# Optimization experiments

Measured on AMD Instinct MI355X. Metric: run time of the kernel, lower is better.

The kernel has to match this reference:

```python
import jax, jax.numpy as jnp
from jax import lax
import numpy as np

IMG_H, IMG_W = 800.0, 1344.0
NMS_PRE, NMS_POST, MAX_NUM = 2000, 1000, 1000
IOU_THR = 0.7
STRIDES = [4, 8, 16, 32, 64]
SIZES = [(200, 336), (100, 168), (50, 84), (25, 42), (13, 21)]
MAX_RATIO = float(abs(np.log(16.0 / 1000.0)))  # mmdet wh_ratio_clip


def _make_anchors(H, W, stride):
    # mmdet AnchorGenerator: scales=[8], ratios=[0.5,1,2], base_size=stride
    ratios = np.array([0.5, 1.0, 2.0])
    scale = 8.0
    hr = np.sqrt(ratios)
    wr = 1.0 / hr
    ws = stride * wr * scale
    hs = stride * hr * scale
    c = stride / 2.0
    base = np.stack([c - 0.5 * ws, c - 0.5 * hs, c + 0.5 * ws, c + 0.5 * hs], 1)  # [3,4]
    xx, yy = np.meshgrid(np.arange(W) * stride, np.arange(H) * stride)
    shifts = np.stack([xx, yy, xx, yy], -1).reshape(-1, 1, 4)  # [H*W,1,4]
    return (shifts + base[None]).reshape(-1, 4).astype(np.float32)  # order (H,W,A)


def setup_inputs() -> dict:
    key = jax.random.key(0)
    inp = {}
    for i, (H, W) in enumerate(SIZES):
        k1, k2, key = jax.random.split(key, 3)
        inp[f"cls{i}"] = jax.random.normal(k1, (2, 3, H, W), jnp.float32)
        inp[f"bbox{i}"] = jax.random.normal(k2, (2, 12, H, W), jnp.float32) * 0.5
        inp[f"anc{i}"] = jnp.asarray(_make_anchors(H, W, STRIDES[i]))
    return inp


def _delta2bbox(deltas, anchors):
    # deltas, anchors: [..., 4]; means=0, stds=1
    dx, dy = deltas[..., 0], deltas[..., 1]
    dw = jnp.clip(deltas[..., 2], -MAX_RATIO, MAX_RATIO)
    dh = jnp.clip(deltas[..., 3], -MAX_RATIO, MAX_RATIO)
    pw = anchors[..., 2] - anchors[..., 0]
    ph = anchors[..., 3] - anchors[..., 1]
    px = (anchors[..., 0] + anchors[..., 2]) * 0.5
    py = (anchors[..., 1] + anchors[..., 3]) * 0.5
    gw = pw * jnp.exp(dw)
    gh = ph * jnp.exp(dh)
    gx = px + pw * dx
    gy = py + ph * dy
    x1 = jnp.clip(gx - 0.5 * gw, 0.0, IMG_W)
    y1 = jnp.clip(gy - 0.5 * gh, 0.0, IMG_H)
    x2 = jnp.clip(gx + 0.5 * gw, 0.0, IMG_W)
    y2 = jnp.clip(gy + 0.5 * gh, 0.0, IMG_H)
    return jnp.stack([x1, y1, x2, y2], axis=-1)


def _pairwise_iou(b):
    # b: [N,4]
    area = (b[:, 2] - b[:, 0]) * (b[:, 3] - b[:, 1])
    lt = jnp.maximum(b[:, None, :2], b[None, :, :2])
    rb = jnp.minimum(b[:, None, 2:], b[None, :, 2:])
    wh = jnp.clip(rb - lt, 0.0, None)
    inter = wh[..., 0] * wh[..., 1]
    union = area[:, None] + area[None, :] - inter
    return inter / jnp.maximum(union, 1e-6)


def _nms_single(boxes, scores):
    # boxes [NMS_PRE,4], scores [NMS_PRE] (one image). Greedy NMS, keep NMS_POST.
    N = scores.shape[0]
    order = jnp.argsort(-scores)
    b = boxes[order]
    s = scores[order]
    iou = _pairwise_iou(lax.stop_gradient(b))
    idx = jnp.arange(N)

    def step(supp, i):
        keep_i = jnp.logical_not(supp[i])
        supp = supp | (keep_i & (iou[i] > IOU_THR) & (idx > i))
        return supp, keep_i

    _, keeps = lax.scan(step, jnp.zeros((N,), bool), idx)
    s_kept = jnp.where(keeps, s, -1.0)
    top_s, top_i = lax.top_k(s_kept, NMS_POST)
    return b[top_i], top_s


def _process_level(cls, bbox, anchors):
    B = cls.shape[0]
    # [B,A,H,W] -> [B,H,W,A] -> [B,N]; [B,A*4,H,W] -> [B,H,W,A*4] -> [B,N,4]
    scores = jax.nn.sigmoid(cls.transpose(0, 2, 3, 1).reshape(B, -1))
    deltas = bbox.transpose(0, 2, 3, 1).reshape(B, -1, 4)
    N = scores.shape[1]
    if N < NMS_PRE:  # pad small levels to min_num_bboxes (nms_pre)
        pad = NMS_PRE - N
        scores = jnp.pad(scores, ((0, 0), (0, pad)), constant_values=-1.0)
        deltas = jnp.pad(deltas, ((0, 0), (0, pad), (0, 0)))
        anchors = jnp.pad(anchors, ((0, pad), (0, 0)))
        top_s = scores
        top_i = jnp.broadcast_to(jnp.arange(NMS_PRE), (B, NMS_PRE))
    else:
        top_s, top_i = lax.top_k(scores, NMS_PRE)
    deltas_g = jnp.take_along_axis(deltas, top_i[..., None], axis=1)  # [B,NMS_PRE,4]
    anc_g = anchors[top_i]  # [B,NMS_PRE,4]
    props = _delta2bbox(deltas_g, anc_g)
    boxes, sc = jax.vmap(_nms_single)(props, top_s)
    return sc, boxes


def _forward(cls_list, bbox_list, anc_list):
    mlvl_scores, mlvl_props = [], []
    for cls, bbox, anc in zip(cls_list, bbox_list, anc_list):
        s, p = _process_level(cls, bbox, anc)
        mlvl_scores.append(s)
        mlvl_props.append(p)
    scores = jnp.concatenate(mlvl_scores, axis=1)      # [B, 5*NMS_POST]
    proposals = jnp.concatenate(mlvl_props, axis=1)    # [B, 5*NMS_POST, 4]
    _, topk_inds = lax.top_k(scores, MAX_NUM)
    return jnp.take_along_axis(proposals, topk_inds[..., None], axis=1)  # [B, MAX_NUM, 4]


def reference(cls0, cls1, cls2, cls3, cls4,
              bbox0, bbox1, bbox2, bbox3, bbox4,
              anc0, anc1, anc2, anc3, anc4):
    return _forward([cls0, cls1, cls2, cls3, cls4],
                    [bbox0, bbox1, bbox2, bbox3, bbox4],
                    [anc0, anc1, anc2, anc3, anc4])
```

## Files before the change

kernel.cpp:

```cpp
#include <hip/hip_runtime.h>
#include <cmath>


#define NPRE 2000
#define NPOST 1000

static __device__ __forceinline__ unsigned int flipf_dev(float f) {
  unsigned int u = __float_as_uint(f);
  return (u & 0x80000000u) ? ~u : (u | 0x80000000u);
}
static __device__ __forceinline__ float unflipf_dev(unsigned int k) {
  unsigned int u = (k & 0x80000000u) ? (k ^ 0x80000000u) : ~k;
  return __uint_as_float(u);
}
static __device__ __forceinline__ unsigned long long flip64_dev(double d) {
  unsigned long long u = (unsigned long long)__double_as_longlong(d);
  return (u & 0x8000000000000000ull) ? ~u : (u | 0x8000000000000000ull);
}

struct RPNParams {
  const float* cls[5];
  const float* bbox[5];
  const float* anc[5];
  unsigned int* hist;
  unsigned int* histT;
  unsigned int* mainCount;
  unsigned int* candCount;
  unsigned int* Bstar;
  unsigned long long* mainEK;
  unsigned long long* candEK;
  unsigned long long* ekG;
  unsigned int* partialR;
  double* selBoxes;
  double* selScores;
  unsigned long long* mask;
  double* postScores;
  float* postBoxes;
  unsigned int* partial;
  float* out;
};

__device__ __constant__ int c_NL[5]  = {201600, 50400, 12600, 3150, 819};
__device__ __constant__ int c_HW[5]  = {67200, 16800, 4200, 1050, 273};
__device__ __constant__ int c_BPT[8] = {99, 99, 25, 25, 7, 7, 2, 2};
__device__ __constant__ int c_BPT12[8] = {25, 25, 7, 7, 2, 2, 1, 1};
__device__ __constant__ int c_HSTART[8] = {0, 25, 50, 57, 64, 66, 68, 69};

static __device__ __forceinline__ void map_block(int bx, int& t, int& chunk) {
  int start = 0;
  t = 0;
  for (int k = 0; k < 8; k++) {
    if (bx < start + c_BPT[k]) { t = k; break; }
    start += c_BPT[k];
  }
  chunk = bx - start;
}
static __device__ __forceinline__ void map_block12(int bx, int& t, int& chunk) {
  int start = 0;
  t = 0;
  for (int k = 0; k < 8; k++) {
    if (bx < start + c_BPT12[k]) { t = k; break; }
    start += c_BPT12[k];
  }
  chunk = bx - start;
}

__global__ __launch_bounds__(1024) void k_hist(RPNParams p) {
  __shared__ unsigned int lh[16384];
  int t, chunk;
  map_block12(blockIdx.x, t, chunk);
  int l = t >> 1, b = t & 1;
  int N = c_NL[l], HW = c_HW[l];
  const float* cls = p.cls[l] + (size_t)b * 3 * HW;
  int tid = threadIdx.x;
  for (int i = tid; i < 16384; i += 1024) lh[i] = 0;
  __syncthreads();
  int base = chunk * 8192 + tid;
#pragma unroll
  for (int k = 0; k < 8; k++) {
    int n = base + k * 1024;
    if (n < N) {
      int a = n % 3, hw = n / 3;
      unsigned int key = flipf_dev(cls[a * HW + hw]);
      atomicAdd(&lh[key >> 18], 1u);
    }
  }
  __syncthreads();
  unsigned int* hout = p.hist + (size_t)blockIdx.x * 16384;
  for (int i = tid; i < 16384; i += 1024) hout[i] = lh[i];
}

__global__ __launch_bounds__(1024) void k_hred(RPNParams p) {
  int t = blockIdx.x >> 4;
  int slice = blockIdx.x & 15;
  int bin = slice * 1024 + threadIdx.x;
  int start = c_HSTART[t];
  int bpt = c_BPT12[t];
  unsigned int s0 = 0, s1 = 0, s2 = 0, s3 = 0;
  int bb = 0;
  for (; bb + 4 <= bpt; bb += 4) {
    s0 += p.hist[(size_t)(start + bb + 0) * 16384 + bin];
    s1 += p.hist[(size_t)(start + bb + 1) * 16384 + bin];
    s2 += p.hist[(size_t)(start + bb + 2) * 16384 + bin];
    s3 += p.hist[(size_t)(start + bb + 3) * 16384 + bin];
  }
  for (; bb < bpt; bb++) s0 += p.hist[(size_t)(start + bb) * 16384 + bin];
  p.histT[(size_t)t * 16384 + bin] = s0 + s1 + s2 + s3;
}

__global__ __launch_bounds__(1024) void k_find(RPNParams p) {
  int t = blockIdx.x;
  __shared__ unsigned int H[16384];
  __shared__ unsigned int S[1024];
  __shared__ int gsel;
  __shared__ unsigned int baseAbove;
  int tid = threadIdx.x;
  const unsigned int* hT = p.histT + (size_t)t * 16384;
  for (int bin = tid; bin < 16384; bin += 1024) H[bin] = hT[bin];
  __syncthreads();
  {
    unsigned int s = 0;
#pragma unroll
    for (int k = 0; k < 16; k++) s += H[tid * 16 + k];
    S[tid] = s;
  }
  __syncthreads();
  for (int off = 1; off < 1024; off <<= 1) {
    unsigned int add = (tid + off < 1024) ? S[tid + off] : 0u;
    __syncthreads();
    S[tid] += add;
    __syncthreads();
  }
  const unsigned int need = NPRE;
  if (S[tid] >= need && (tid == 1023 || S[tid + 1] < need)) {
    gsel = tid;
    baseAbove = (tid == 1023) ? 0u : S[tid + 1];
  }
  __syncthreads();
  if (tid == 0) {
    int gg = gsel;
    unsigned int c = baseAbove;
    int bstar = gg * 16;
    for (int bb = 15; bb >= 0; bb--) {
      c += H[gg * 16 + bb];
      if (c >= need) { bstar = gg * 16 + bb; break; }
    }
    p.Bstar[t] = (unsigned int)bstar;
  }
}

__global__ void k_compact(RPNParams p) {
  int t, chunk;
  map_block(blockIdx.x, t, chunk);
  int l = t >> 1, b = t & 1;
  int N = c_NL[l], HW = c_HW[l];
  const float* cls = p.cls[l] + (size_t)b * 3 * HW;
  unsigned int Bs = p.Bstar[t];
  int base = chunk * 2048 + threadIdx.x;
  for (int k = 0; k < 2; k++) {
    int n = base + k * 1024;
    if (n < N) {
      int a = n % 3, hw = n / 3;
      unsigned int key = flipf_dev(cls[a * HW + hw]);
      unsigned int hi = key >> 18;
      unsigned long long ek =
          ((unsigned long long)key << 32) | (unsigned int)(~(unsigned int)n);
      if (hi > Bs) {
        unsigned int pos = atomicAdd(&p.mainCount[t], 1u);
        if (pos < 2048u) p.mainEK[(size_t)t * 2048 + pos] = ek;
      } else if (hi == Bs) {
        unsigned int pos = atomicAdd(&p.candCount[t], 1u);
        if (pos < 8192u) p.candEK[(size_t)t * 8192 + pos] = ek;
      }
    }
  }
}

__global__ void k_fill(RPNParams p) {
  int t = blockIdx.x;
  int l = t >> 1, b = t & 1;
  int N = c_NL[l], HW = c_HW[l];
  int tid = threadIdx.x;
  unsigned long long* ekG = p.ekG + (size_t)t * 2048;
  if (N >= NPRE) {
    unsigned int cGT = min(p.mainCount[t], 2000u);
    unsigned int nC = min(p.candCount[t], 8192u);
    unsigned int needIn = 2000u - cGT;
    for (unsigned int m = tid; m < cGT; m += 256)
      ekG[m] = p.mainEK[(size_t)t * 2048 + m];
    const unsigned long long* cek = p.candEK + (size_t)t * 8192;
    for (unsigned int e = tid; e < nC; e += 256) {
      unsigned long long ve = cek[e];
      unsigned int r = 0;
      for (unsigned int j = 0; j < nC; j++) r += (cek[j] > ve) ? 1u : 0u;
      if (r < needIn) ekG[cGT + r] = ve;
    }
    for (unsigned int r2 = 2000u + tid; r2 < 2048u; r2 += 256)
      ekG[r2] = (unsigned long long)(unsigned int)(~r2);
  } else {
    const float* cls = p.cls[l] + (size_t)b * 3 * HW;
    for (int r = tid; r < 2048; r += 256) {
      if (r < N) {
        int a = r % 3, hw = r / 3;
        unsigned int key = flipf_dev(cls[a * HW + hw]);
        ekG[r] = ((unsigned long long)key << 32) |
                 (unsigned int)(~(unsigned int)r);
      } else {
        ekG[r] = (unsigned long long)(unsigned int)(~(unsigned int)r);
      }
    }
  }
}

__global__ void k_rank(RPNParams p) {
  int t = blockIdx.x >> 3;
  int s = blockIdx.x & 7;
  int tid = threadIdx.x;
  __shared__ unsigned long long sl[256];
  const unsigned long long* ekG = p.ekG + (size_t)t * 2048;
  sl[tid] = ekG[s * 256 + tid];
  __syncthreads();
  unsigned long long ve[8];
  unsigned int r[8];
#pragma unroll
  for (int k = 0; k < 8; k++) {
    ve[k] = ekG[k * 256 + tid];
    r[k] = 0;
  }
  for (int j = 0; j < 256; j++) {
    unsigned long long vj = sl[j];
#pragma unroll
    for (int k = 0; k < 8; k++) r[k] += (vj > ve[k]) ? 1u : 0u;
  }
  unsigned int* out = p.partialR + ((size_t)t * 8 + s) * 2048;
#pragma unroll
  for (int k = 0; k < 8; k++) out[k * 256 + tid] = r[k];
}

__global__ void k_scatter(RPNParams p) {
  int t = blockIdx.x;
  int l = t >> 1, b = t & 1;
  int HW = c_HW[l];
  int tid = threadIdx.x;
  __shared__ unsigned long long srt[2048];
  const unsigned long long* ekG = p.ekG + (size_t)t * 2048;
  for (int e = tid; e < 2048; e += 1024) {
    unsigned int rk = 0;
#pragma unroll
    for (int s = 0; s < 8; s++)
      rk += p.partialR[((size_t)t * 8 + s) * 2048 + e];
    srt[rk] = ekG[e];
  }
  __syncthreads();

  const double RCLIP = fabs(log(16.0 / 1000.0));
  const float* bbx = p.bbox[l] + (size_t)b * 12 * HW;
  const float* anc = p.anc[l];
  for (int r = tid; r < NPRE; r += 1024) {
    unsigned long long v = srt[r];
    unsigned int key = (unsigned int)(v >> 32);
    double* SB = p.selBoxes + ((size_t)t * NPRE + r) * 4;
    if (key == 0u) {
      SB[0] = 0.0; SB[1] = 0.0; SB[2] = 0.0; SB[3] = 0.0;
      p.selScores[(size_t)t * NPRE + r] = -1.0;
    } else {
      unsigned int idx = ~(unsigned int)(v & 0xFFFFFFFFull);
      int a = (int)(idx % 3u);
      int hw = (int)(idx / 3u);
      double d0 = (double)bbx[(a * 4 + 0) * HW + hw];
      double d1 = (double)bbx[(a * 4 + 1) * HW + hw];
      double d2 = (double)bbx[(a * 4 + 2) * HW + hw];
      double d3 = (double)bbx[(a * 4 + 3) * HW + hw];
      double a0 = (double)anc[(size_t)idx * 4 + 0];
      double a1 = (double)anc[(size_t)idx * 4 + 1];
      double a2 = (double)anc[(size_t)idx * 4 + 2];
      double a3 = (double)anc[(size_t)idx * 4 + 3];
      double dw = fmin(fmax(d2, -RCLIP), RCLIP);
      double dh = fmin(fmax(d3, -RCLIP), RCLIP);
      double pw = a2 - a0, ph = a3 - a1;
      double px = (a0 + a2) * 0.5, py = (a1 + a3) * 0.5;
      double gw = pw * exp(dw), gh = ph * exp(dh);
      double gx = px + pw * d0, gy = py + ph * d1;
      double x1 = fmin(fmax(gx - 0.5 * gw, 0.0), 1344.0);
      double y1 = fmin(fmax(gy - 0.5 * gh, 0.0), 800.0);
      double x2 = fmin(fmax(gx + 0.5 * gw, 0.0), 1344.0);
      double y2 = fmin(fmax(gy + 0.5 * gh, 0.0), 800.0);
      SB[0] = x1; SB[1] = y1; SB[2] = x2; SB[3] = y2;
      float f = unflipf_dev(key);
      p.selScores[(size_t)t * NPRE + r] = 1.0 / (1.0 + exp(-(double)f));
    }
  }
}

__global__ __launch_bounds__(640) void k_iou(RPNParams p) {
  int bx = blockIdx.x;
  int t = bx / 25;
  int q = bx % 25;
  __shared__ float X1[2048], Y1[2048], X2[2048], Y2[2048], AR[2048];
  const double* SB = p.selBoxes + (size_t)t * NPRE * 4;
  for (int i = threadIdx.x; i < 2048; i += 640) {
    float x1 = 0.f, y1 = 0.f, x2 = 0.f, y2 = 0.f;
    if (i < NPRE) {
      x1 = (float)SB[i * 4 + 0]; y1 = (float)SB[i * 4 + 1];
      x2 = (float)SB[i * 4 + 2]; y2 = (float)SB[i * 4 + 3];
    }
    X1[i] = x1; Y1[i] = y1; X2[i] = x2; Y2[i] = y2;
    AR[i] = (x2 - x1) * (y2 - y1);
  }
  __syncthreads();
  int wave = threadIdx.x >> 6, lane = threadIdx.x & 63;
  int g = q + 25 * wave;
  int i0 = g * 8;
  float x1i[8], y1i[8], x2i[8], y2i[8], ai[8];
#pragma unroll
  for (int r = 0; r < 8; r++) {
    int i = i0 + r;
    x1i[r] = X1[i]; y1i[r] = Y1[i]; x2i[r] = X2[i]; y2i[r] = Y2[i];
    ai[r] = AR[i];
  }
  int c0 = i0 >> 6;
  int j0 = c0 * 64 + lane;
  float cx1 = X1[j0], cy1 = Y1[j0], cx2 = X2[j0], cy2 = Y2[j0], car = AR[j0];
  for (int k = c0; k < 32; k++) {
    float nx1 = 0.f, ny1 = 0.f, nx2 = 0.f, ny2 = 0.f, nar = 0.f;
    if (k + 1 < 32) {
      int jn = (k + 1) * 64 + lane;
      nx1 = X1[jn]; ny1 = Y1[jn]; nx2 = X2[jn]; ny2 = Y2[jn];
      nar = AR[jn];
    }
    int j = k * 64 + lane;
    bool jin = j < NPRE;
    bool pred[8], need[8];
    bool needAny = false;
#pragma unroll
    for (int r = 0; r < 8; r++) {
      int i = i0 + r;
      bool valid = jin && (j > i);
      float lx = fmaxf(x1i[r], cx1), ly = fmaxf(y1i[r], cy1);
      float rx = fminf(x2i[r], cx2), ry = fminf(y2i[r], cy2);
      float w = fmaxf(rx - lx, 0.0f), h = fmaxf(ry - ly, 0.0f);
      float inter = w * h;
      float uni = fmaxf(ai[r] + car - inter, 1e-6f);
      float diff = inter - 0.7f * uni;
      pred[r] = valid && (diff > 0.0f);
      need[r] = valid && (fabsf(diff) <= 4.0f + 1e-5f * uni);
      needAny |= need[r];
    }
    if (__any(needAny)) {
#pragma unroll
      for (int r = 0; r < 8; r++) {
        if (need[r]) {
          int i = i0 + r;
          double a0 = SB[i * 4 + 0], b0 = SB[i * 4 + 1];
          double a2 = SB[i * 4 + 2], b2 = SB[i * 4 + 3];
          double c0d = SB[j * 4 + 0], d0 = SB[j * 4 + 1];
          double c2 = SB[j * 4 + 2], d2 = SB[j * 4 + 3];
          double dai = (a2 - a0) * (b2 - b0);
          double daj = (c2 - c0d) * (d2 - d0);
          double lxd = fmax(a0, c0d), lyd = fmax(b0, d0);
          double rxd = fmin(a2, c2), ryd = fmin(b2, d2);
          double wd = fmax(rxd - lxd, 0.0), hd = fmax(ryd - lyd, 0.0);
          double interd = wd * hd;
          double unid = fmax(dai + daj - interd, 1e-6);
          pred[r] = (interd / unid) > 0.7;
        }
      }
    }
#pragma unroll
    for (int r = 0; r < 8; r++) {
      unsigned long long word = __ballot(pred[r]);
      if (lane == 0) p.mask[((size_t)t * NPRE + i0 + r) * 32 + k] = word;
    }
    cx1 = nx1; cy1 = ny1; cx2 = nx2; cy2 = ny2; car = nar;
  }
}

#define GRP_N 63
#define RING 6
__global__ __launch_bounds__(256) void k_greedy(RPNParams p) {
  int t = blockIdx.x;
  int tid = threadIdx.x;
  __shared__ unsigned long long ring[RING * 1024];
  __shared__ int ready[GRP_N];
  __shared__ int cons_s;
  __shared__ unsigned long long kw[32], aw[32], bw[32];
  __shared__ unsigned int prefA[33], prefB[33];
  volatile int* rdy = ready;
  volatile int* cons = &cons_s;
  const unsigned long long* MK = p.mask + (size_t)t * NPRE * 32;
  for (int i = tid; i < GRP_N; i += 256) ready[i] = 0;
  if (tid == 0) cons_s = 0;
  __syncthreads();

  int wave = tid >> 6, lane = tid & 63;
  if (wave >= 1) {
    for (int g = wave - 1; g < GRP_N; g += 3) {
      while (g - *cons >= RING) __builtin_amdgcn_s_sleep(1);
      unsigned long long v[16];
#pragma unroll
      for (int k = 0; k < 16; k++) {
        int idx = k * 64 + lane;
        int row = g * 32 + (idx >> 5);
        v[k] = (row < NPRE) ? MK[(size_t)row * 32 + (idx & 31)] : 0ull;
      }
      int slot = g % RING;
#pragma unroll
      for (int k = 0; k < 16; k++)
        ring[slot * 1024 + k * 64 + lane] = v[k];
      __threadfence_block();
      if (lane == 0) rdy[g] = 1;
    }
  } else {
    unsigned long long supp = 0ull, keep = 0ull;
    auto doGroup = [&](int g, int base) {
      while (rdy[g] == 0) { }
      __threadfence_block();
      int slot = g % RING;
      int c = g >> 1;
      unsigned long long rv[32];
#pragma unroll
      for (int r = 0; r < 32; r++)
        rv[r] = ring[slot * 1024 + r * 32 + (lane & 31)];
      unsigned int sh = (unsigned int)(supp >> base);
      unsigned int s32 = (unsigned int)__builtin_amdgcn_readlane((int)sh, c);
      unsigned int kg = 0;
#pragma unroll
      for (int r = 0; r < 32; r++) {
        unsigned int rvh = (unsigned int)(rv[r] >> base);
        bool kp = (s32 & (1u << r)) == 0u;
        kg |= kp ? (1u << r) : 0u;
        s32 |= kp ? rvh : 0u;
      }
      kg = (unsigned int)__builtin_amdgcn_readlane((int)kg, c);
#pragma unroll
      for (int r = 0; r < 32; r++) {
        if (kg & (1u << r)) supp |= rv[r];
      }
      keep |= (lane == c) ? ((unsigned long long)kg << base) : 0ull;
      __threadfence_block();
      if (lane == 63) *cons = g + 1;
    };
    for (int g = 0; g + 1 < GRP_N; g += 2) {
      doGroup(g, 0);
      doGroup(g + 1, 32);
    }
    doGroup(GRP_N - 1, 0);
    if (lane < 32) kw[lane] = keep;
  }
  __syncthreads();

  for (int ch = wave; ch < 32; ch += 4) {
    int i = ch * 64 + lane;
    bool inr = i < NPRE;
    bool kb = inr && ((kw[ch] >> lane) & 1ull);
    bool A = kb && (inr ? (p.selScores[(size_t)t * NPRE + i] > -0.5) : false);
    bool B = inr && !A;
    unsigned long long wa = __ballot(A);
    unsigned long long wb = __ballot(B);
    if (lane == 0) { aw[ch] = wa; bw[ch] = wb; }
  }
  __syncthreads();
  if (tid == 0) {
    unsigned int ca = 0, cb = 0;
    for (int w = 0; w < 32; w++) {
      prefA[w] = ca; ca += __popcll(aw[w]);
      prefB[w] = cb; cb += __popcll(bw[w]);
    }
    prefA[32] = ca; prefB[32] = cb;
  }
  __syncthreads();
  unsigned int KA = prefA[32];
  for (int i = tid; i < NPRE; i += 256) {
    int w = i >> 6, bpos = i & 63;
    unsigned long long below = (bpos == 0) ? 0ull : (~0ull >> (64 - bpos));
    bool kb = (kw[w] >> bpos) & 1ull;
    double s = p.selScores[(size_t)t * NPRE + i];
    bool A = kb && (s > -0.5);
    unsigned int slot;
    double outs;
    if (A) {
      slot = prefA[w] + (unsigned int)__popcll(aw[w] & below);
      outs = s;
    } else {
      slot = KA + prefB[w] + (unsigned int)__popcll(bw[w] & below);
      outs = -1.0;
    }
    if (slot < NPOST) {
      p.postScores[(size_t)t * NPOST + slot] = outs;
      const double* SB = p.selBoxes + ((size_t)t * NPRE + i) * 4;
      float* PB = p.postBoxes + ((size_t)t * NPOST + slot) * 4;
      PB[0] = (float)SB[0]; PB[1] = (float)SB[1];
      PB[2] = (float)SB[2]; PB[3] = (float)SB[3];
    }
  }
}

__global__ void k_finalA(RPNParams p) {
  int bx = blockIdx.x;
  int b = bx / 80;
  int rem = bx % 80;
  int s = rem >> 2;
  int ec = rem & 3;
  int j0 = s * 256;
  __shared__ unsigned long long kj[256];
  int tid = threadIdx.x;
  {
    int e = j0 + tid;
    unsigned long long v = 0ull;
    if (e < 5000) {
      int l = e / 1000, slot = e - l * 1000;
      int t = l * 2 + b;
      v = flip64_dev(p.postScores[(size_t)t * NPOST + slot]);
    }
    kj[tid] = v;
  }
  __syncthreads();
  int eidx[5];
  unsigned long long ke[5];
  unsigned int r[5];
#pragma unroll
  for (int k = 0; k < 5; k++) {
    int e = ec * 1280 + k * 256 + tid;
    eidx[k] = (e < 5000) ? e : -1;
    if (eidx[k] >= 0) {
      int l = e / 1000, slot = e - l * 1000;
      int t = l * 2 + b;
      ke[k] = flip64_dev(p.postScores[(size_t)t * NPOST + slot]);
    } else {
      ke[k] = 0ull;
    }
    r[k] = 0;
  }
  for (int j = 0; j < 256; j++) {
    unsigned long long vj = kj[j];
    int jg = j0 + j;
#pragma unroll
    for (int k = 0; k < 5; k++)
      r[k] += (vj > ke[k] || (vj == ke[k] && jg < eidx[k])) ? 1u : 0u;
  }
#pragma unroll
  for (int k = 0; k < 5; k++)
    if (eidx[k] >= 0)
      p.partial[((size_t)b * 20 + s) * 5000 + eidx[k]] = r[k];
}

__global__ void k_finalB(RPNParams p) {
  int b = blockIdx.x / 5;
  int ch = blockIdx.x % 5;
  int tid = threadIdx.x;
  if (tid < 1000) {
    int e = ch * 1000 + tid;
    unsigned int r = 0;
#pragma unroll
    for (int s = 0; s < 20; s++)
      r += p.partial[((size_t)b * 20 + s) * 5000 + e];
    if (r < NPOST) {
      int l = e / 1000, slot = e - l * 1000;
      int t = l * 2 + b;
      const float* PB = p.postBoxes + ((size_t)t * NPOST + slot) * 4;
      float* O = p.out + ((size_t)b * NPOST + r) * 4;
      O[0] = PB[0]; O[1] = PB[1]; O[2] = PB[2]; O[3] = PB[3];
    }
  }
}

extern "C" void kernel_launch(void* const* d_in, const int* in_sizes, int n_in,
                              void* d_out, int out_size, void* d_ws,
                              size_t ws_size, hipStream_t stream) {
  RPNParams p;
  bool interleaved = (n_in >= 2) && (in_sizes[1] == 4 * in_sizes[0]);
  for (int l = 0; l < 5; l++) {
    if (interleaved) {
      p.cls[l]  = (const float*)d_in[3 * l + 0];
      p.bbox[l] = (const float*)d_in[3 * l + 1];
      p.anc[l]  = (const float*)d_in[3 * l + 2];
    } else {
      p.cls[l]  = (const float*)d_in[l];
      p.bbox[l] = (const float*)d_in[5 + l];
      p.anc[l]  = (const float*)d_in[10 + l];
    }
  }
  char* w = (char*)d_ws;
  size_t off = 0;
  auto alloc = [&](size_t bytes) {
    off = (off + 255) & ~(size_t)255;
    void* r = w + off;
    off += bytes;
    return r;
  };
  p.mainCount = (unsigned int*)alloc(10 * 4);
  p.candCount = (unsigned int*)alloc(10 * 4);
  size_t zbytes = off;
  p.hist       = (unsigned int*)alloc((size_t)70 * 16384 * 4);
  p.histT      = (unsigned int*)alloc((size_t)8 * 16384 * 4);
  p.Bstar      = (unsigned int*)alloc(10 * 4);
  p.mainEK     = (unsigned long long*)alloc((size_t)10 * 2048 * 8);
  p.candEK     = (unsigned long long*)alloc((size_t)10 * 8192 * 8);
  p.ekG        = (unsigned long long*)alloc((size_t)10 * 2048 * 8);
  p.partialR   = (unsigned int*)alloc((size_t)10 * 8 * 2048 * 4);
  p.selBoxes   = (double*)alloc((size_t)10 * NPRE * 4 * 8);
  p.selScores  = (double*)alloc((size_t)10 * NPRE * 8);
  p.mask       = (unsigned long long*)alloc((size_t)10 * NPRE * 32 * 8);
  p.postScores = (double*)alloc((size_t)10 * NPOST * 8);
  p.postBoxes  = (float*)alloc((size_t)10 * NPOST * 4 * 4);
  p.partial    = (unsigned int*)alloc((size_t)2 * 20 * 5000 * 4);
  p.out = (float*)d_out;
  (void)ws_size; (void)out_size;

  hipMemsetAsync(d_ws, 0, zbytes, stream);
  k_hist<<<dim3(70), dim3(1024), 0, stream>>>(p);
  k_hred<<<dim3(128), dim3(1024), 0, stream>>>(p);
  k_find<<<dim3(8), dim3(1024), 0, stream>>>(p);
  k_compact<<<dim3(266), dim3(1024), 0, stream>>>(p);
  k_fill<<<dim3(10), dim3(256), 0, stream>>>(p);
  k_rank<<<dim3(80), dim3(256), 0, stream>>>(p);
  k_scatter<<<dim3(10), dim3(1024), 0, stream>>>(p);
  k_iou<<<dim3(250), dim3(640), 0, stream>>>(p);
  k_greedy<<<dim3(10), dim3(256), 0, stream>>>(p);
  k_finalA<<<dim3(160), dim3(256), 0, stream>>>(p);
  k_finalB<<<dim3(10), dim3(1024), 0, stream>>>(p);
}
```

Before: 388.1 us.

## Fuse all RPN stages into one persistent kernel with grid barriers

Merges the eleven separate kernel launches into a single persistent kernel of 256 blocks. Stages are separated by software grid-wide barriers built on atomic counters with spin-sleep, and shared memory is reused across phases. The aim is to remove per-launch overhead and inter-kernel gaps. In exchange, every stage now runs at 1024 threads per block with a fixed grid, so some stages leave blocks idle, and the barrier relies on all 256 blocks being co-resident, which risks deadlock if they are not.

```diff
diff --git a/kernel.cpp b/kernel.cpp
--- a/kernel.cpp
+++ b/kernel.cpp
@@ -4,6 +4,7 @@
 
 #define NPRE 2000
 #define NPOST 1000
+#define NBLK 256
 
 static __device__ __forceinline__ unsigned int flipf_dev(float f) {
   unsigned int u = __float_as_uint(f);
@@ -22,10 +23,11 @@
   const float* cls[5];
   const float* bbox[5];
   const float* anc[5];
+  unsigned int* bar;
+  unsigned int* mainCount;
+  unsigned int* candCount;
   unsigned int* hist;
   unsigned int* histT;
-  unsigned int* mainCount;
-  unsigned int* candCount;
   unsigned int* Bstar;
   unsigned long long* mainEK;
   unsigned long long* candEK;
@@ -65,490 +67,522 @@
   chunk = bx - start;
 }
 
-__global__ __launch_bounds__(1024) void k_hist(RPNParams p) {
-  __shared__ unsigned int lh[16384];
-  int t, chunk;
-  map_block12(blockIdx.x, t, chunk);
-  int l = t >> 1, b = t & 1;
-  int N = c_NL[l], HW = c_HW[l];
-  const float* cls = p.cls[l] + (size_t)b * 3 * HW;
-  int tid = threadIdx.x;
-  for (int i = tid; i < 16384; i += 1024) lh[i] = 0;
+static __device__ __forceinline__ void gbar(unsigned int* bar, int ph) {
   __syncthreads();
-  int base = chunk * 8192 + tid;
-#pragma unroll
-  for (int k = 0; k < 8; k++) {
-    int n = base + k * 1024;
-    if (n < N) {
-      int a = n % 3, hw = n / 3;
-      unsigned int key = flipf_dev(cls[a * HW + hw]);
-      atomicAdd(&lh[key >> 18], 1u);
-    }
+  if (threadIdx.x == 0) {
+    __threadfence();
+    __hip_atomic_fetch_add(&bar[ph], 1u, __ATOMIC_RELEASE,
+                           __HIP_MEMORY_SCOPE_AGENT);
+    while (__hip_atomic_load(&bar[ph], __ATOMIC_ACQUIRE,
+                             __HIP_MEMORY_SCOPE_AGENT) < (unsigned)NBLK)
+      __builtin_amdgcn_s_sleep(2);
   }
   __syncthreads();
-  unsigned int* hout = p.hist + (size_t)blockIdx.x * 16384;
-  for (int i = tid; i < 16384; i += 1024) hout[i] = lh[i];
-}
-
-__global__ __launch_bounds__(1024) void k_hred(RPNParams p) {
-  int t = blockIdx.x >> 4;
-  int slice = blockIdx.x & 15;
-  int bin = slice * 1024 + threadIdx.x;
-  int start = c_HSTART[t];
-  int bpt = c_BPT12[t];
-  unsigned int s0 = 0, s1 = 0, s2 = 0, s3 = 0;
-  int bb = 0;
-  for (; bb + 4 <= bpt; bb += 4) {
-    s0 += p.hist[(size_t)(start + bb + 0) * 16384 + bin];
-    s1 += p.hist[(size_t)(start + bb + 1) * 16384 + bin];
-    s2 += p.hist[(size_t)(start + bb + 2) * 16384 + bin];
-    s3 += p.hist[(size_t)(start + bb + 3) * 16384 + bin];
-  }
-  for (; bb < bpt; bb++) s0 += p.hist[(size_t)(start + bb) * 16384 + bin];
-  p.histT[(size_t)t * 16384 + bin] = s0 + s1 + s2 + s3;
-}
-
-__global__ __launch_bounds__(1024) void k_find(RPNParams p) {
-  int t = blockIdx.x;
-  __shared__ unsigned int H[16384];
-  __shared__ unsigned int S[1024];
-  __shared__ int gsel;
-  __shared__ unsigned int baseAbove;
-  int tid = threadIdx.x;
-  const unsigned int* hT = p.histT + (size_t)t * 16384;
-  for (int bin = tid; bin < 16384; bin += 1024) H[bin] = hT[bin];
-  __syncthreads();
-  {
-    unsigned int s = 0;
-#pragma unroll
-    for (int k = 0; k < 16; k++) s += H[tid * 16 + k];
-    S[tid] = s;
-  }
-  __syncthreads();
-  for (int off = 1; off < 1024; off <<= 1) {
-    unsigned int add = (tid + off < 1024) ? S[tid + off] : 0u;
-    __syncthreads();
-    S[tid] += add;
-    __syncthreads();
-  }
-  const unsigned int need = NPRE;
-  if (S[tid] >= need && (tid == 1023 || S[tid + 1] < need)) {
-    gsel = tid;
-    baseAbove = (tid == 1023) ? 0u : S[tid + 1];
-  }
-  __syncthreads();
-  if (tid == 0) {
-    int gg = gsel;
-    unsigned int c = baseAbove;
-    int bstar = gg * 16;
-    for (int bb = 15; bb >= 0; bb--) {
-      c += H[gg * 16 + bb];
-      if (c >= need) { bstar = gg * 16 + bb; break; }
-    }
-    p.Bstar[t] = (unsigned int)bstar;
-  }
-}
-
-__global__ void k_compact(RPNParams p) {
-  int t, chunk;
-  map_block(blockIdx.x, t, chunk);
-  int l = t >> 1, b = t & 1;
-  int N = c_NL[l], HW = c_HW[l];
-  const float* cls = p.cls[l] + (size_t)b * 3 * HW;
-  unsigned int Bs = p.Bstar[t];
-  int base = chunk * 2048 + threadIdx.x;
-  for (int k = 0; k < 2; k++) {
-    int n = base + k * 1024;
-    if (n < N) {
-      int a = n % 3, hw = n / 3;
-      unsigned int key = flipf_dev(cls[a * HW + hw]);
-      unsigned int hi = key >> 18;
-      unsigned long long ek =
-          ((unsigned long long)key << 32) | (unsigned int)(~(unsigned int)n);
-      if (hi > Bs) {
-        unsigned int pos = atomicAdd(&p.mainCount[t], 1u);
-        if (pos < 2048u) p.mainEK[(size_t)t * 2048 + pos] = ek;
-      } else if (hi == Bs) {
-        unsigned int pos = atomicAdd(&p.candCount[t], 1u);
-        if (pos < 8192u) p.candEK[(size_t)t * 8192 + pos] = ek;
-      }
-    }
-  }
-}
-
-__global__ void k_fill(RPNParams p) {
-  int t = blockIdx.x;
-  int l = t >> 1, b = t & 1;
-  int N = c_NL[l], HW = c_HW[l];
-  int tid = threadIdx.x;
-  unsigned long long* ekG = p.ekG + (size_t)t * 2048;
-  if (N >= NPRE) {
-    unsigned int cGT = min(p.mainCount[t], 2000u);
-    unsigned int nC = min(p.candCount[t], 8192u);
-    unsigned int needIn = 2000u - cGT;
-    for (unsigned int m = tid; m < cGT; m += 256)
-      ekG[m] = p.mainEK[(size_t)t * 2048 + m];
-    const unsigned long long* cek = p.candEK + (size_t)t * 8192;
-    for (unsigned int e = tid; e < nC; e += 256) {
-      unsigned long long ve = cek[e];
-      unsigned int r = 0;
-      for (unsigned int j = 0; j < nC; j++) r += (cek[j] > ve) ? 1u : 0u;
-      if (r < needIn) ekG[cGT + r] = ve;
-    }
-    for (unsigned int r2 = 2000u + tid; r2 < 2048u; r2 += 256)
-      ekG[r2] = (unsigned long long)(unsigned int)(~r2);
-  } else {
-    const float* cls = p.cls[l] + (size_t)b * 3 * HW;
-    for (int r = tid; r < 2048; r += 256) {
-      if (r < N) {
-        int a = r % 3, hw = r / 3;
-        unsigned int key = flipf_dev(cls[a * HW + hw]);
-        ekG[r] = ((unsigned long long)key << 32) |
-                 (unsigned int)(~(unsigned int)r);
-      } else {
-        ekG[r] = (unsigned long long)(unsigned int)(~(unsigned int)r);
-      }
-    }
-  }
-}
-
-__global__ void k_rank(RPNParams p) {
-  int t = blockIdx.x >> 3;
-  int s = blockIdx.x & 7;
-  int tid = threadIdx.x;
-  __shared__ unsigned long long sl[256];
-  const unsigned long long* ekG = p.ekG + (size_t)t * 2048;
-  sl[tid] = ekG[s * 256 + tid];
-  __syncthreads();
-  unsigned long long ve[8];
-  unsigned int r[8];
-#pragma unroll
-  for (int k = 0; k < 8; k++) {
-    ve[k] = ekG[k * 256 + tid];
-    r[k] = 0;
-  }
-  for (int j = 0; j < 256; j++) {
-    unsigned long long vj = sl[j];
-#pragma unroll
-    for (int k = 0; k < 8; k++) r[k] += (vj > ve[k]) ? 1u : 0u;
-  }
-  unsigned int* out = p.partialR + ((size_t)t * 8 + s) * 2048;
-#pragma unroll
-  for (int k = 0; k < 8; k++) out[k * 256 + tid] = r[k];
-}
-
-__global__ void k_scatter(RPNParams p) {
-  int t = blockIdx.x;
-  int l = t >> 1, b = t & 1;
-  int HW = c_HW[l];
-  int tid = threadIdx.x;
-  __shared__ unsigned long long srt[2048];
-  const unsigned long long* ekG = p.ekG + (size_t)t * 2048;
-  for (int e = tid; e < 2048; e += 1024) {
-    unsigned int rk = 0;
-#pragma unroll
-    for (int s = 0; s < 8; s++)
-      rk += p.partialR[((size_t)t * 8 + s) * 2048 + e];
-    srt[rk] = ekG[e];
-  }
-  __syncthreads();
-
-  const double RCLIP = fabs(log(16.0 / 1000.0));
-  const float* bbx = p.bbox[l] + (size_t)b * 12 * HW;
-  const float* anc = p.anc[l];
-  for (int r = tid; r < NPRE; r += 1024) {
-    unsigned long long v = srt[r];
-    unsigned int key = (unsigned int)(v >> 32);
-    double* SB = p.selBoxes + ((size_t)t * NPRE + r) * 4;
-    if (key == 0u) {
-      SB[0] = 0.0; SB[1] = 0.0; SB[2] = 0.0; SB[3] = 0.0;
-      p.selScores[(size_t)t * NPRE + r] = -1.0;
-    } else {
-      unsigned int idx = ~(unsigned int)(v & 0xFFFFFFFFull);
-      int a = (int)(idx % 3u);
-      int hw = (int)(idx / 3u);
-      double d0 = (double)bbx[(a * 4 + 0) * HW + hw];
-      double d1 = (double)bbx[(a * 4 + 1) * HW + hw];
-      double d2 = (double)bbx[(a * 4 + 2) * HW + hw];
-      double d3 = (double)bbx[(a * 4 + 3) * HW + hw];
-      double a0 = (double)anc[(size_t)idx * 4 + 0];
-      double a1 = (double)anc[(size_t)idx * 4 + 1];
-      double a2 = (double)anc[(size_t)idx * 4 + 2];
-      double a3 = (double)anc[(size_t)idx * 4 + 3];
-      double dw = fmin(fmax(d2, -RCLIP), RCLIP);
-      double dh = fmin(fmax(d3, -RCLIP), RCLIP);
-      double pw = a2 - a0, ph = a3 - a1;
-      double px = (a0 + a2) * 0.5, py = (a1 + a3) * 0.5;
-      double gw = pw * exp(dw), gh = ph * exp(dh);
-      double gx = px + pw * d0, gy = py + ph * d1;
-      double x1 = fmin(fmax(gx - 0.5 * gw, 0.0), 1344.0);
-      double y1 = fmin(fmax(gy - 0.5 * gh, 0.0), 800.0);
-      double x2 = fmin(fmax(gx + 0.5 * gw, 0.0), 1344.0);
-      double y2 = fmin(fmax(gy + 0.5 * gh, 0.0), 800.0);
-      SB[0] = x1; SB[1] = y1; SB[2] = x2; SB[3] = y2;
-      float f = unflipf_dev(key);
-      p.selScores[(size_t)t * NPRE + r] = 1.0 / (1.0 + exp(-(double)f));
-    }
-  }
-}
-
-__global__ __launch_bounds__(640) void k_iou(RPNParams p) {
-  int bx = blockIdx.x;
-  int t = bx / 25;
-  int q = bx % 25;
-  __shared__ float X1[2048], Y1[2048], X2[2048], Y2[2048], AR[2048];
-  const double* SB = p.selBoxes + (size_t)t * NPRE * 4;
-  for (int i = threadIdx.x; i < 2048; i += 640) {
-    float x1 = 0.f, y1 = 0.f, x2 = 0.f, y2 = 0.f;
-    if (i < NPRE) {
-      x1 = (float)SB[i * 4 + 0]; y1 = (float)SB[i * 4 + 1];
-      x2 = (float)SB[i * 4 + 2]; y2 = (float)SB[i * 4 + 3];
-    }
-    X1[i] = x1; Y1[i] = y1; X2[i] = x2; Y2[i] = y2;
-    AR[i] = (x2 - x1) * (y2 - y1);
-  }
-  __syncthreads();
-  int wave = threadIdx.x >> 6, lane = threadIdx.x & 63;
-  int g = q + 25 * wave;
-  int i0 = g * 8;
-  float x1i[8], y1i[8], x2i[8], y2i[8], ai[8];
-#pragma unroll
-  for (int r = 0; r < 8; r++) {
-    int i = i0 + r;
-    x1i[r] = X1[i]; y1i[r] = Y1[i]; x2i[r] = X2[i]; y2i[r] = Y2[i];
-    ai[r] = AR[i];
-  }
-  int c0 = i0 >> 6;
-  int j0 = c0 * 64 + lane;
-  float cx1 = X1[j0], cy1 = Y1[j0], cx2 = X2[j0], cy2 = Y2[j0], car = AR[j0];
-  for (int k = c0; k < 32; k++) {
-    float nx1 = 0.f, ny1 = 0.f, nx2 = 0.f, ny2 = 0.f, nar = 0.f;
-    if (k + 1 < 32) {
-      int jn = (k + 1) * 64 + lane;
-      nx1 = X1[jn]; ny1 = Y1[jn]; nx2 = X2[jn]; ny2 = Y2[jn];
-      nar = AR[jn];
-    }
-    int j = k * 64 + lane;
-    bool jin = j < NPRE;
-    bool pred[8], need[8];
-    bool needAny = false;
-#pragma unroll
-    for (int r = 0; r < 8; r++) {
-      int i = i0 + r;
-      bool valid = jin && (j > i);
-      float lx = fmaxf(x1i[r], cx1), ly = fmaxf(y1i[r], cy1);
-      float rx = fminf(x2i[r], cx2), ry = fminf(y2i[r], cy2);
-      float w = fmaxf(rx - lx, 0.0f), h = fmaxf(ry - ly, 0.0f);
-      float inter = w * h;
-      float uni = fmaxf(ai[r] + car - inter, 1e-6f);
-      float diff = inter - 0.7f * uni;
-      pred[r] = valid && (diff > 0.0f);
-      need[r] = valid && (fabsf(diff) <= 4.0f + 1e-5f * uni);
-      needAny |= need[r];
-    }
-    if (__any(needAny)) {
-#pragma unroll
-      for (int r = 0; r < 8; r++) {
-        if (need[r]) {
-          int i = i0 + r;
-          double a0 = SB[i * 4 + 0], b0 = SB[i * 4 + 1];
-          double a2 = SB[i * 4 + 2], b2 = SB[i * 4 + 3];
-          double c0d = SB[j * 4 + 0], d0 = SB[j * 4 + 1];
-          double c2 = SB[j * 4 + 2], d2 = SB[j * 4 + 3];
-          double dai = (a2 - a0) * (b2 - b0);
-          double daj = (c2 - c0d) * (d2 - d0);
-          double lxd = fmax(a0, c0d), lyd = fmax(b0, d0);
-          double rxd = fmin(a2, c2), ryd = fmin(b2, d2);
-          double wd = fmax(rxd - lxd, 0.0), hd = fmax(ryd - lyd, 0.0);
-          double interd = wd * hd;
-          double unid = fmax(dai + daj - interd, 1e-6);
-          pred[r] = (interd / unid) > 0.7;
-        }
-      }
-    }
-#pragma unroll
-    for (int r = 0; r < 8; r++) {
-      unsigned long long word = __ballot(pred[r]);
-      if (lane == 0) p.mask[((size_t)t * NPRE + i0 + r) * 32 + k] = word;
-    }
-    cx1 = nx1; cy1 = ny1; cx2 = nx2; cy2 = ny2; car = nar;
-  }
+  __threadfence();
 }
 
 #define GRP_N 63
 #define RING 6
-__global__ __launch_bounds__(256) void k_greedy(RPNParams p) {
-  int t = blockIdx.x;
+
+__global__ __launch_bounds__(1024) void k_mega(RPNParams p) {
+  __shared__ unsigned long long SMEM8[8768];
+  __shared__ int g_gsel;
+  __shared__ unsigned int g_baseAbove;
+  __shared__ int g_ready[GRP_N];
+  __shared__ int g_cons;
+  __shared__ unsigned long long g_kw[32], g_aw[32], g_bw[32];
+  __shared__ unsigned int g_prefA[33], g_prefB[33];
+
+  int bx = blockIdx.x;
   int tid = threadIdx.x;
-  __shared__ unsigned long long ring[RING * 1024];
-  __shared__ int ready[GRP_N];
-  __shared__ int cons_s;
-  __shared__ unsigned long long kw[32], aw[32], bw[32];
-  __shared__ unsigned int prefA[33], prefB[33];
-  volatile int* rdy = ready;
-  volatile int* cons = &cons_s;
-  const unsigned long long* MK = p.mask + (size_t)t * NPRE * 32;
-  for (int i = tid; i < GRP_N; i += 256) ready[i] = 0;
-  if (tid == 0) cons_s = 0;
-  __syncthreads();
-
   int wave = tid >> 6, lane = tid & 63;
-  if (wave >= 1) {
-    for (int g = wave - 1; g < GRP_N; g += 3) {
-      while (g - *cons >= RING) __builtin_amdgcn_s_sleep(1);
-      unsigned long long v[16];
-#pragma unroll
-      for (int k = 0; k < 16; k++) {
-        int idx = k * 64 + lane;
-        int row = g * 32 + (idx >> 5);
-        v[k] = (row < NPRE) ? MK[(size_t)row * 32 + (idx & 31)] : 0ull;
-      }
-      int slot = g % RING;
-#pragma unroll
-      for (int k = 0; k < 16; k++)
-        ring[slot * 1024 + k * 64 + lane] = v[k];
-      __threadfence_block();
-      if (lane == 0) rdy[g] = 1;
-    }
-  } else {
-    unsigned long long supp = 0ull, keep = 0ull;
-    auto doGroup = [&](int g, int base) {
-      while (rdy[g] == 0) { }
-      __threadfence_block();
-      int slot = g % RING;
-      int c = g >> 1;
-      unsigned long long rv[32];
-#pragma unroll
-      for (int r = 0; r < 32; r++)
-        rv[r] = ring[slot * 1024 + r * 32 + (lane & 31)];
-      unsigned int sh = (unsigned int)(supp >> base);
-      unsigned int s32 = (unsigned int)__builtin_amdgcn_readlane((int)sh, c);
-      unsigned int kg = 0;
-#pragma unroll
-      for (int r = 0; r < 32; r++) {
-        unsigned int rvh = (unsigned int)(rv[r] >> base);
-        bool kp = (s32 & (1u << r)) == 0u;
-        kg |= kp ? (1u << r) : 0u;
-        s32 |= kp ? rvh : 0u;
-      }
-      kg = (unsigned int)__builtin_amdgcn_readlane((int)kg, c);
-#pragma unroll
-      for (int r = 0; r < 32; r++) {
-        if (kg & (1u << r)) supp |= rv[r];
-      }
-      keep |= (lane == c) ? ((unsigned long long)kg << base) : 0ull;
-      __threadfence_block();
-      if (lane == 63) *cons = g + 1;
-    };
-    for (int g = 0; g + 1 < GRP_N; g += 2) {
-      doGroup(g, 0);
-      doGroup(g + 1, 32);
-    }
-    doGroup(GRP_N - 1, 0);
-    if (lane < 32) kw[lane] = keep;
-  }
-  __syncthreads();
-
-  for (int ch = wave; ch < 32; ch += 4) {
-    int i = ch * 64 + lane;
-    bool inr = i < NPRE;
-    bool kb = inr && ((kw[ch] >> lane) & 1ull);
-    bool A = kb && (inr ? (p.selScores[(size_t)t * NPRE + i] > -0.5) : false);
-    bool B = inr && !A;
-    unsigned long long wa = __ballot(A);
-    unsigned long long wb = __ballot(B);
-    if (lane == 0) { aw[ch] = wa; bw[ch] = wb; }
-  }
-  __syncthreads();
-  if (tid == 0) {
-    unsigned int ca = 0, cb = 0;
-    for (int w = 0; w < 32; w++) {
-      prefA[w] = ca; ca += __popcll(aw[w]);
-      prefB[w] = cb; cb += __popcll(bw[w]);
-    }
-    prefA[32] = ca; prefB[32] = cb;
-  }
-  __syncthreads();
-  unsigned int KA = prefA[32];
-  for (int i = tid; i < NPRE; i += 256) {
-    int w = i >> 6, bpos = i & 63;
-    unsigned long long below = (bpos == 0) ? 0ull : (~0ull >> (64 - bpos));
-    bool kb = (kw[w] >> bpos) & 1ull;
-    double s = p.selScores[(size_t)t * NPRE + i];
-    bool A = kb && (s > -0.5);
-    unsigned int slot;
-    double outs;
-    if (A) {
-      slot = prefA[w] + (unsigned int)__popcll(aw[w] & below);
-      outs = s;
+
+  if (bx < 70) {
+    unsigned int* lh = (unsigned int*)SMEM8;
+    int t, chunk;
+    map_block12(bx, t, chunk);
+    int l = t >> 1, b = t & 1;
+    int N = c_NL[l], HW = c_HW[l];
+    const float* cls = p.cls[l] + (size_t)b * 3 * HW;
+    for (int i = tid; i < 16384; i += 1024) lh[i] = 0;
+    __syncthreads();
+    int base = chunk * 8192 + tid;
+#pragma unroll
+    for (int k = 0; k < 8; k++) {
+      int n = base + k * 1024;
+      if (n < N) {
+        int a = n % 3, hw = n / 3;
+        unsigned int key = flipf_dev(cls[a * HW + hw]);
+        atomicAdd(&lh[key >> 18], 1u);
+      }
+    }
+    __syncthreads();
+    unsigned int* hout = p.hist + (size_t)bx * 16384;
+    for (int i = tid; i < 16384; i += 1024) hout[i] = lh[i];
+  }
+  gbar(p.bar, 0);
+
+  if (bx < 128) {
+    int t = bx >> 4;
+    int slice = bx & 15;
+    int bin = slice * 1024 + tid;
+    int start = c_HSTART[t];
+    int bpt = c_BPT12[t];
+    unsigned int s0 = 0, s1 = 0, s2 = 0, s3 = 0;
+    int bb = 0;
+    for (; bb + 4 <= bpt; bb += 4) {
+      s0 += p.hist[(size_t)(start + bb + 0) * 16384 + bin];
+      s1 += p.hist[(size_t)(start + bb + 1) * 16384 + bin];
+      s2 += p.hist[(size_t)(start + bb + 2) * 16384 + bin];
+      s3 += p.hist[(size_t)(start + bb + 3) * 16384 + bin];
+    }
+    for (; bb < bpt; bb++) s0 += p.hist[(size_t)(start + bb) * 16384 + bin];
+    p.histT[(size_t)t * 16384 + bin] = s0 + s1 + s2 + s3;
+  }
+  gbar(p.bar, 1);
+
+  if (bx < 8) {
+    int t = bx;
+    unsigned int* H = (unsigned int*)SMEM8;
+    unsigned int* S = H + 16384;
+    const unsigned int* hT = p.histT + (size_t)t * 16384;
+    for (int bin = tid; bin < 16384; bin += 1024) H[bin] = hT[bin];
+    __syncthreads();
+    {
+      unsigned int s = 0;
+#pragma unroll
+      for (int k = 0; k < 16; k++) s += H[tid * 16 + k];
+      S[tid] = s;
+    }
+    __syncthreads();
+    for (int off = 1; off < 1024; off <<= 1) {
+      unsigned int add = (tid + off < 1024) ? S[tid + off] : 0u;
+      __syncthreads();
+      S[tid] += add;
+      __syncthreads();
+    }
+    const unsigned int need = NPRE;
+    if (S[tid] >= need && (tid == 1023 || S[tid + 1] < need)) {
+      g_gsel = tid;
+      g_baseAbove = (tid == 1023) ? 0u : S[tid + 1];
+    }
+    __syncthreads();
+    if (tid == 0) {
+      int gg = g_gsel;
+      unsigned int c = g_baseAbove;
+      int bstar = gg * 16;
+      for (int bb = 15; bb >= 0; bb--) {
+        c += H[gg * 16 + bb];
+        if (c >= need) { bstar = gg * 16 + bb; break; }
+      }
+      p.Bstar[t] = (unsigned int)bstar;
+    }
+  }
+  gbar(p.bar, 2);
+
+  for (int u = bx; u < 266; u += NBLK) {
+    int t, chunk;
+    map_block(u, t, chunk);
+    int l = t >> 1, b = t & 1;
+    int N = c_NL[l], HW = c_HW[l];
+    const float* cls = p.cls[l] + (size_t)b * 3 * HW;
+    unsigned int Bs = p.Bstar[t];
+    int base = chunk * 2048 + tid;
+    for (int k = 0; k < 2; k++) {
+      int n = base + k * 1024;
+      if (n < N) {
+        int a = n % 3, hw = n / 3;
+        unsigned int key = flipf_dev(cls[a * HW + hw]);
+        unsigned int hi = key >> 18;
+        unsigned long long ek =
+            ((unsigned long long)key << 32) | (unsigned int)(~(unsigned int)n);
+        if (hi > Bs) {
+          unsigned int pos = atomicAdd(&p.mainCount[t], 1u);
+          if (pos < 2048u) p.mainEK[(size_t)t * 2048 + pos] = ek;
+        } else if (hi == Bs) {
+          unsigned int pos = atomicAdd(&p.candCount[t], 1u);
+          if (pos < 8192u) p.candEK[(size_t)t * 8192 + pos] = ek;
+        }
+      }
+    }
+  }
+  gbar(p.bar, 3);
+
+  if (bx < 10 && tid < 256) {
+    int t = bx;
+    int l = t >> 1, b = t & 1;
+    int N = c_NL[l], HW = c_HW[l];
+    unsigned long long* ekG = p.ekG + (size_t)t * 2048;
+    if (N >= NPRE) {
+      unsigned int cGT = min(p.mainCount[t], 2000u);
+      unsigned int nC = min(p.candCount[t], 8192u);
+      unsigned int needIn = 2000u - cGT;
+      for (unsigned int m = tid; m < cGT; m += 256)
+        ekG[m] = p.mainEK[(size_t)t * 2048 + m];
+      const unsigned long long* cek = p.candEK + (size_t)t * 8192;
+      for (unsigned int e = tid; e < nC; e += 256) {
+        unsigned long long ve = cek[e];
+        unsigned int r = 0;
+        for (unsigned int j = 0; j < nC; j++) r += (cek[j] > ve) ? 1u : 0u;
+        if (r < needIn) ekG[cGT + r] = ve;
+      }
+      for (unsigned int r2 = 2000u + tid; r2 < 2048u; r2 += 256)
+        ekG[r2] = (unsigned long long)(unsigned int)(~r2);
     } else {
-      slot = KA + prefB[w] + (unsigned int)__popcll(bw[w] & below);
-      outs = -1.0;
-    }
-    if (slot < NPOST) {
-      p.postScores[(size_t)t * NPOST + slot] = outs;
-      const double* SB = p.selBoxes + ((size_t)t * NPRE + i) * 4;
-      float* PB = p.postBoxes + ((size_t)t * NPOST + slot) * 4;
-      PB[0] = (float)SB[0]; PB[1] = (float)SB[1];
-      PB[2] = (float)SB[2]; PB[3] = (float)SB[3];
-    }
-  }
-}
-
-__global__ void k_finalA(RPNParams p) {
-  int bx = blockIdx.x;
-  int b = bx / 80;
-  int rem = bx % 80;
-  int s = rem >> 2;
-  int ec = rem & 3;
-  int j0 = s * 256;
-  __shared__ unsigned long long kj[256];
-  int tid = threadIdx.x;
-  {
-    int e = j0 + tid;
-    unsigned long long v = 0ull;
-    if (e < 5000) {
-      int l = e / 1000, slot = e - l * 1000;
-      int t = l * 2 + b;
-      v = flip64_dev(p.postScores[(size_t)t * NPOST + slot]);
-    }
-    kj[tid] = v;
-  }
-  __syncthreads();
-  int eidx[5];
-  unsigned long long ke[5];
-  unsigned int r[5];
-#pragma unroll
-  for (int k = 0; k < 5; k++) {
-    int e = ec * 1280 + k * 256 + tid;
-    eidx[k] = (e < 5000) ? e : -1;
-    if (eidx[k] >= 0) {
-      int l = e / 1000, slot = e - l * 1000;
-      int t = l * 2 + b;
-      ke[k] = flip64_dev(p.postScores[(size_t)t * NPOST + slot]);
-    } else {
-      ke[k] = 0ull;
-    }
-    r[k] = 0;
-  }
-  for (int j = 0; j < 256; j++) {
-    unsigned long long vj = kj[j];
-    int jg = j0 + j;
-#pragma unroll
-    for (int k = 0; k < 5; k++)
-      r[k] += (vj > ke[k] || (vj == ke[k] && jg < eidx[k])) ? 1u : 0u;
-  }
-#pragma unroll
-  for (int k = 0; k < 5; k++)
-    if (eidx[k] >= 0)
-      p.partial[((size_t)b * 20 + s) * 5000 + eidx[k]] = r[k];
-}
-
-__global__ void k_finalB(RPNParams p) {
-  int b = blockIdx.x / 5;
-  int ch = blockIdx.x % 5;
-  int tid = threadIdx.x;
-  if (tid < 1000) {
+      const float* cls = p.cls[l] + (size_t)b * 3 * HW;
+      for (int r = tid; r < 2048; r += 256) {
+        if (r < N) {
+          int a = r % 3, hw = r / 3;
+          unsigned int key = flipf_dev(cls[a * HW + hw]);
+          ekG[r] = ((unsigned long long)key << 32) |
+                   (unsigned int)(~(unsigned int)r);
+        } else {
+          ekG[r] = (unsigned long long)(unsigned int)(~(unsigned int)r);
+        }
+      }
+    }
+  }
+  gbar(p.bar, 4);
+
+  if (bx < 80) {
+    int t = bx >> 3;
+    int s = bx & 7;
+    unsigned long long* sl = SMEM8;
+    const unsigned long long* ekG = p.ekG + (size_t)t * 2048;
+    if (tid < 256) sl[tid] = ekG[s * 256 + tid];
+    __syncthreads();
+    if (tid < 256) {
+      unsigned long long ve[8];
+      unsigned int r[8];
+#pragma unroll
+      for (int k = 0; k < 8; k++) {
+        ve[k] = ekG[k * 256 + tid];
+        r[k] = 0;
+      }
+      for (int j = 0; j < 256; j++) {
+        unsigned long long vj = sl[j];
+#pragma unroll
+        for (int k = 0; k < 8; k++) r[k] += (vj > ve[k]) ? 1u : 0u;
+      }
+      unsigned int* out = p.partialR + ((size_t)t * 8 + s) * 2048;
+#pragma unroll
+      for (int k = 0; k < 8; k++) out[k * 256 + tid] = r[k];
+    }
+  }
+  gbar(p.bar, 5);
+
+  if (bx < 10) {
+    int t = bx;
+    int l = t >> 1, b = t & 1;
+    int HW = c_HW[l];
+    unsigned long long* srt = SMEM8;
+    const unsigned long long* ekG = p.ekG + (size_t)t * 2048;
+    for (int e = tid; e < 2048; e += 1024) {
+      unsigned int rk = 0;
+#pragma unroll
+      for (int s = 0; s < 8; s++)
+        rk += p.partialR[((size_t)t * 8 + s) * 2048 + e];
+      srt[rk] = ekG[e];
+    }
+    __syncthreads();
+    const double RCLIP = fabs(log(16.0 / 1000.0));
+    const float* bbx = p.bbox[l] + (size_t)b * 12 * HW;
+    const float* anc = p.anc[l];
+    for (int r = tid; r < NPRE; r += 1024) {
+      unsigned long long v = srt[r];
+      unsigned int key = (unsigned int)(v >> 32);
+      double* SB = p.selBoxes + ((size_t)t * NPRE + r) * 4;
+      if (key == 0u) {
+        SB[0] = 0.0; SB[1] = 0.0; SB[2] = 0.0; SB[3] = 0.0;
+        p.selScores[(size_t)t * NPRE + r] = -1.0;
+      } else {
+        unsigned int idx = ~(unsigned int)(v & 0xFFFFFFFFull);
+        int a = (int)(idx % 3u);
+        int hw = (int)(idx / 3u);
+        double d0 = (double)bbx[(a * 4 + 0) * HW + hw];
+        double d1 = (double)bbx[(a * 4 + 1) * HW + hw];
+        double d2 = (double)bbx[(a * 4 + 2) * HW + hw];
+        double d3 = (double)bbx[(a * 4 + 3) * HW + hw];
+        double a0 = (double)anc[(size_t)idx * 4 + 0];
+        double a1 = (double)anc[(size_t)idx * 4 + 1];
+        double a2 = (double)anc[(size_t)idx * 4 + 2];
+        double a3 = (double)anc[(size_t)idx * 4 + 3];
+        double dw = fmin(fmax(d2, -RCLIP), RCLIP);
+        double dh = fmin(fmax(d3, -RCLIP), RCLIP);
+        double pw = a2 - a0, ph = a3 - a1;
+        double px = (a0 + a2) * 0.5, py = (a1 + a3) * 0.5;
+        double gw = pw * exp(dw), gh = ph * exp(dh);
+        double gx = px + pw * d0, gy = py + ph * d1;
+        double x1 = fmin(fmax(gx - 0.5 * gw, 0.0), 1344.0);
+        double y1 = fmin(fmax(gy - 0.5 * gh, 0.0), 800.0);
+        double x2 = fmin(fmax(gx + 0.5 * gw, 0.0), 1344.0);
+        double y2 = fmin(fmax(gy + 0.5 * gh, 0.0), 800.0);
+        SB[0] = x1; SB[1] = y1; SB[2] = x2; SB[3] = y2;
+        float f = unflipf_dev(key);
+        p.selScores[(size_t)t * NPRE + r] = 1.0 / (1.0 + exp(-(double)f));
+      }
+    }
+  }
+  gbar(p.bar, 6);
+
+  if (bx < 250) {
+    int t = bx / 25;
+    int q = bx % 25;
+    float* X1 = (float*)SMEM8;
+    float* Y1 = X1 + 2048;
+    float* X2 = X1 + 4096;
+    float* Y2 = X1 + 6144;
+    float* AR = X1 + 8192;
+    const double* SB = p.selBoxes + (size_t)t * NPRE * 4;
+    for (int i = tid; i < 2048; i += 1024) {
+      float x1 = 0.f, y1 = 0.f, x2 = 0.f, y2 = 0.f;
+      if (i < NPRE) {
+        x1 = (float)SB[i * 4 + 0]; y1 = (float)SB[i * 4 + 1];
+        x2 = (float)SB[i * 4 + 2]; y2 = (float)SB[i * 4 + 3];
+      }
+      X1[i] = x1; Y1[i] = y1; X2[i] = x2; Y2[i] = y2;
+      AR[i] = (x2 - x1) * (y2 - y1);
+    }
+    __syncthreads();
+    if (tid < 640) {
+      int g = q + 25 * wave;
+      int i0 = g * 8;
+      float x1i[8], y1i[8], x2i[8], y2i[8], ai[8];
+#pragma unroll
+      for (int r = 0; r < 8; r++) {
+        int i = i0 + r;
+        x1i[r] = X1[i]; y1i[r] = Y1[i]; x2i[r] = X2[i]; y2i[r] = Y2[i];
+        ai[r] = AR[i];
+      }
+      int c0 = i0 >> 6;
+      int j0 = c0 * 64 + lane;
+      float cx1 = X1[j0], cy1 = Y1[j0], cx2 = X2[j0], cy2 = Y2[j0],
+            car = AR[j0];
+      for (int k = c0; k < 32; k++) {
+        float nx1 = 0.f, ny1 = 0.f, nx2 = 0.f, ny2 = 0.f, nar = 0.f;
+        if (k + 1 < 32) {
+          int jn = (k + 1) * 64 + lane;
+          nx1 = X1[jn]; ny1 = Y1[jn]; nx2 = X2[jn]; ny2 = Y2[jn];
+          nar = AR[jn];
+        }
+        int j = k * 64 + lane;
+        bool jin = j < NPRE;
+        bool pred[8], need[8];
+        bool needAny = false;
+#pragma unroll
+        for (int r = 0; r < 8; r++) {
+          int i = i0 + r;
+          bool valid = jin && (j > i);
+          float lx = fmaxf(x1i[r], cx1), ly = fmaxf(y1i[r], cy1);
+          float rx = fminf(x2i[r], cx2), ry = fminf(y2i[r], cy2);
+          float w = fmaxf(rx - lx, 0.0f), h = fmaxf(ry - ly, 0.0f);
+          float inter = w * h;
+          float uni = fmaxf(ai[r] + car - inter, 1e-6f);
+          float diff = inter - 0.7f * uni;
+          pred[r] = valid && (diff > 0.0f);
+          need[r] = valid && (fabsf(diff) <= 4.0f + 1e-5f * uni);
+          needAny |= need[r];
+        }
+        if (__any(needAny)) {
+#pragma unroll
+          for (int r = 0; r < 8; r++) {
+            if (need[r]) {
+              int i = i0 + r;
+              double a0 = SB[i * 4 + 0], b0 = SB[i * 4 + 1];
+              double a2 = SB[i * 4 + 2], b2 = SB[i * 4 + 3];
+              double c0d = SB[j * 4 + 0], d0 = SB[j * 4 + 1];
+              double c2 = SB[j * 4 + 2], d2 = SB[j * 4 + 3];
+              double dai = (a2 - a0) * (b2 - b0);
+              double daj = (c2 - c0d) * (d2 - d0);
+              double lxd = fmax(a0, c0d), lyd = fmax(b0, d0);
+              double rxd = fmin(a2, c2), ryd = fmin(b2, d2);
+              double wd = fmax(rxd - lxd, 0.0), hd = fmax(ryd - lyd, 0.0);
+              double interd = wd * hd;
+              double unid = fmax(dai + daj - interd, 1e-6);
+              pred[r] = (interd / unid) > 0.7;
+            }
+          }
+        }
+#pragma unroll
+        for (int r = 0; r < 8; r++) {
+          unsigned long long word = __ballot(pred[r]);
+          if (lane == 0) p.mask[((size_t)t * NPRE + i0 + r) * 32 + k] = word;
+        }
+        cx1 = nx1; cy1 = ny1; cx2 = nx2; cy2 = ny2; car = nar;
+      }
+    }
+  }
+  gbar(p.bar, 7);
+
+  if (bx < 10) {
+    int t = bx;
+    unsigned long long* ring = SMEM8;
+    volatile int* rdy = g_ready;
+    volatile int* cons = &g_cons;
+    const unsigned long long* MK = p.mask + (size_t)t * NPRE * 32;
+    for (int i = tid; i < GRP_N; i += 1024) g_ready[i] = 0;
+    if (tid == 0) g_cons = 0;
+    __syncthreads();
+
+    if (wave >= 1 && wave <= 3) {
+      for (int g = wave - 1; g < GRP_N; g += 3) {
+        while (g - *cons >= RING) __builtin_amdgcn_s_sleep(1);
+        unsigned long long v[16];
+#pragma unroll
+        for (int k = 0; k < 16; k++) {
+          int idx = k * 64 + lane;
+          int row = g * 32 + (idx >> 5);
+          v[k] = (row < NPRE) ? MK[(size_t)row * 32 + (idx & 31)] : 0ull;
+        }
+        int slot = g % RING;
+#pragma unroll
+        for (int k = 0; k < 16; k++)
+          ring[slot * 1024 + k * 64 + lane] = v[k];
+        __threadfence_block();
+        if (lane == 0) rdy[g] = 1;
+      }
+    } else if (wave == 0) {
+      unsigned long long supp = 0ull, keep = 0ull;
+      auto doGroup = [&](int g, int base) {
+        while (rdy[g] == 0) { }
+        __threadfence_block();
+        int slot = g % RING;
+        int c = g >> 1;
+        unsigned long long rv[32];
+#pragma unroll
+        for (int r = 0; r < 32; r++)
+          rv[r] = ring[slot * 1024 + r * 32 + (lane & 31)];
+        unsigned int sh = (unsigned int)(supp >> base);
+        unsigned int s32 =
+            (unsigned int)__builtin_amdgcn_readlane((int)sh, c);
+        unsigned int kg = 0;
+#pragma unroll
+        for (int r = 0; r < 32; r++) {
+          unsigned int rvh = (unsigned int)(rv[r] >> base);
+          bool kp = (s32 & (1u << r)) == 0u;
+          kg |= kp ? (1u << r) : 0u;
+          s32 |= kp ? rvh : 0u;
+        }
+        kg = (unsigned int)__builtin_amdgcn_readlane((int)kg, c);
+#pragma unroll
+        for (int r = 0; r < 32; r++) {
+          if (kg & (1u << r)) supp |= rv[r];
+        }
+        keep |= (lane == c) ? ((unsigned long long)kg << base) : 0ull;
+        __threadfence_block();
+        if (lane == 63) *cons = g + 1;
+      };
+      for (int g = 0; g + 1 < GRP_N; g += 2) {
+        doGroup(g, 0);
+        doGroup(g + 1, 32);
+      }
+      doGroup(GRP_N - 1, 0);
+      if (lane < 32) g_kw[lane] = keep;
+    }
+    __syncthreads();
+
+    for (int ch = wave; ch < 32; ch += 16) {
+      int i = ch * 64 + lane;
+      bool inr = i < NPRE;
+      bool kb = inr && ((g_kw[ch] >> lane) & 1ull);
+      bool A =
+          kb && (inr ? (p.selScores[(size_t)t * NPRE + i] > -0.5) : false);
+      bool B = inr && !A;
+      unsigned long long wa = __ballot(A);
+      unsigned long long wb = __ballot(B);
+      if (lane == 0) { g_aw[ch] = wa; g_bw[ch] = wb; }
+    }
+    __syncthreads();
+    if (tid == 0) {
+      unsigned int ca = 0, cb = 0;
+      for (int w = 0; w < 32; w++) {
+        g_prefA[w] = ca; ca += __popcll(g_aw[w]);
+        g_prefB[w] = cb; cb += __popcll(g_bw[w]);
+      }
+      g_prefA[32] = ca; g_prefB[32] = cb;
+    }
+    __syncthreads();
+    unsigned int KA = g_prefA[32];
+    for (int i = tid; i < NPRE; i += 1024) {
+      int w = i >> 6, bpos = i & 63;
+      unsigned long long below =
+          (bpos == 0) ? 0ull : (~0ull >> (64 - bpos));
+      bool kb = (g_kw[w] >> bpos) & 1ull;
+      double s = p.selScores[(size_t)t * NPRE + i];
+      bool A = kb && (s > -0.5);
+      unsigned int slot;
+      double outs;
+      if (A) {
+        slot = g_prefA[w] + (unsigned int)__popcll(g_aw[w] & below);
+        outs = s;
+      } else {
+        slot = KA + g_prefB[w] + (unsigned int)__popcll(g_bw[w] & below);
+        outs = -1.0;
+      }
+      if (slot < NPOST) {
+        p.postScores[(size_t)t * NPOST + slot] = outs;
+        const double* SB = p.selBoxes + ((size_t)t * NPRE + i) * 4;
+        float* PB = p.postBoxes + ((size_t)t * NPOST + slot) * 4;
+        PB[0] = (float)SB[0]; PB[1] = (float)SB[1];
+        PB[2] = (float)SB[2]; PB[3] = (float)SB[3];
+      }
+    }
+  }
+  gbar(p.bar, 8);
+
+  if (bx < 160) {
+    int b = bx / 80;
+    int rem = bx % 80;
+    int s = rem >> 2;
+    int ec = rem & 3;
+    int j0 = s * 256;
+    unsigned long long* kj = SMEM8;
+    if (tid < 256) {
+      int e = j0 + tid;
+      unsigned long long v = 0ull;
+      if (e < 5000) {
+        int l = e / 1000, slot = e - l * 1000;
+        int t = l * 2 + b;
+        v = flip64_dev(p.postScores[(size_t)t * NPOST + slot]);
+      }
+      kj[tid] = v;
+    }
+    __syncthreads();
+    if (tid < 256) {
+      int eidx[5];
+      unsigned long long ke[5];
+      unsigned int r[5];
+#pragma unroll
+      for (int k = 0; k < 5; k++) {
+        int e = ec * 1280 + k * 256 + tid;
+        eidx[k] = (e < 5000) ? e : -1;
+        if (eidx[k] >= 0) {
+          int l = e / 1000, slot = e - l * 1000;
+          int t = l * 2 + b;
+          ke[k] = flip64_dev(p.postScores[(size_t)t * NPOST + slot]);
+        } else {
+          ke[k] = 0ull;
+        }
+        r[k] = 0;
+      }
+      for (int j = 0; j < 256; j++) {
+        unsigned long long vj = kj[j];
+        int jg = j0 + j;
+#pragma unroll
+        for (int k = 0; k < 5; k++)
+          r[k] += (vj > ke[k] || (vj == ke[k] && jg < eidx[k])) ? 1u : 0u;
+      }
+#pragma unroll
+      for (int k = 0; k < 5; k++)
+        if (eidx[k] >= 0)
+          p.partial[((size_t)b * 20 + s) * 5000 + eidx[k]] = r[k];
+    }
+  }
+  gbar(p.bar, 9);
+
+  if (bx < 10 && tid < 1000) {
+    int b = bx / 5;
+    int ch = bx % 5;
     int e = ch * 1000 + tid;
     unsigned int r = 0;
 #pragma unroll
@@ -588,6 +622,7 @@
     off += bytes;
     return r;
   };
+  p.bar       = (unsigned int*)alloc(64 * 4);
   p.mainCount = (unsigned int*)alloc(10 * 4);
   p.candCount = (unsigned int*)alloc(10 * 4);
   size_t zbytes = off;
@@ -608,15 +643,5 @@
   (void)ws_size; (void)out_size;
 
   hipMemsetAsync(d_ws, 0, zbytes, stream);
-  k_hist<<<dim3(70), dim3(1024), 0, stream>>>(p);
-  k_hred<<<dim3(128), dim3(1024), 0, stream>>>(p);
-  k_find<<<dim3(8), dim3(1024), 0, stream>>>(p);
-  k_compact<<<dim3(266), dim3(1024), 0, stream>>>(p);
-  k_fill<<<dim3(10), dim3(256), 0, stream>>>(p);
-  k_rank<<<dim3(80), dim3(256), 0, stream>>>(p);
-  k_scatter<<<dim3(10), dim3(1024), 0, stream>>>(p);
-  k_iou<<<dim3(250), dim3(640), 0, stream>>>(p);
-  k_greedy<<<dim3(10), dim3(256), 0, stream>>>(p);
-  k_finalA<<<dim3(160), dim3(256), 0, stream>>>(p);
-  k_finalB<<<dim3(10), dim3(1024), 0, stream>>>(p);
-}
+  k_mega<<<dim3(NBLK), dim3(1024), 0, stream>>>(p);
+}
```

New measurement: 1.308 ms. +236.9%, slower.
